# Kernel tuning notes

Hardware: AMD Instinct MI355X
Metric: run time of the kernel (lower is better)

The kernel has to match this reference:

```python
import jax, jax.numpy as jnp
import numpy as np

B, C, N, K, H = 8, 32, 4096, 32, 4  # batch, d_model, num_points, knn, heads
D = C // H
LN_EPS = 1e-5
ATT_EPS = 1e-6


def setup_inputs() -> dict:
    key = jax.random.key(0)
    ks = jax.random.split(key, 12)
    s = 0.05
    return {
        "search_feat": jax.random.normal(ks[0], (B, C, N), jnp.float32),
        "search_xyz": jax.random.normal(ks[1], (B, N, 3), jnp.float32),
        # pos MLP: Linear(3,32)+ReLU+Linear(32,32), weights stored [in,out]
        "w_pos1": jax.random.normal(ks[2], (3, 32), jnp.float32) * s,
        "b_pos1": jnp.zeros((32,), jnp.float32),
        "w_pos2": jax.random.normal(ks[3], (32, 32), jnp.float32) * s,
        "b_pos2": jnp.zeros((32,), jnp.float32),
        "w_q": jax.random.normal(ks[4], (C, C), jnp.float32) * s,
        "w_k": jax.random.normal(ks[5], (C, C), jnp.float32) * s,
        "w_v": jax.random.normal(ks[6], (C, C), jnp.float32) * s,
        "w_merge": jax.random.normal(ks[7], (C, C), jnp.float32) * s,
        "ln1_g": jnp.ones((C,), jnp.float32),
        "ln1_b": jnp.zeros((C,), jnp.float32),
        "w_mlp1": jax.random.normal(ks[8], (2 * C, 2 * C), jnp.float32) * s,
        "w_mlp2": jax.random.normal(ks[9], (2 * C, C), jnp.float32) * s,
        "ln2_g": jnp.ones((C,), jnp.float32),
        "ln2_b": jnp.zeros((C,), jnp.float32),
    }


def _layernorm(x, g, b):
    m = jnp.mean(x, axis=-1, keepdims=True)
    v = jnp.mean((x - m) ** 2, axis=-1, keepdims=True)
    return g * (x - m) * jax.lax.rsqrt(v + LN_EPS) + b


def _elu1(x):
    return jax.nn.elu(x) + 1.0


def reference(search_feat, search_xyz, w_pos1, b_pos1, w_pos2, b_pos2,
              w_q, w_k, w_v, w_merge, ln1_g, ln1_b, w_mlp1, w_mlp2,
              ln2_g, ln2_b):
    b, c, n = search_feat.shape
    h, d, k = H, C // H, K

    xt = jnp.transpose(search_feat, (0, 2, 1))  # [B,N,C]
    # knn in feature space: pd = -||xi||^2 + 2 xi.xj - ||xj||^2 (neg sq dist)
    xx = jnp.sum(xt * xt, axis=-1)  # [B,N]
    pd = 2.0 * jnp.einsum('bnc,bmc->bnm', xt, xt) - xx[:, :, None] - xx[:, None, :]
    idx = jax.lax.top_k(pd, k)[1]  # [B,N,K] nearest (incl. self)

    gather = jax.vmap(lambda f, i: f[i])  # per-batch gather
    fea_knn = gather(xt, idx)            # [B,N,K,C]
    xyz_knn = gather(search_xyz, idx)    # [B,N,K,3]

    def pos_mlp(z):
        return jax.nn.relu(z @ w_pos1 + b_pos1) @ w_pos2 + b_pos2

    q_in = xt + pos_mlp(search_xyz)      # [B,N,C]  (query, L=1)
    kv_in = fea_knn + pos_mlp(xyz_knn)   # [B,N,K,C]

    Q = (q_in @ w_q).reshape(b, n, h, d)          # [B,N,H,D]
    Ky = (kv_in @ w_k).reshape(b, n, k, h, d)     # [B,N,K,H,D]
    V = (kv_in @ w_v).reshape(b, n, k, h, d)

    Qf = _elu1(Q)
    Kf = _elu1(Ky)
    Vn = V / k  # v_length = K
    KV = jnp.einsum('bnkhd,bnkhv->bnhdv', Kf, Vn)
    Z = 1.0 / (jnp.einsum('bnhd,bnhd->bnh', Qf, Kf.sum(axis=2)) + ATT_EPS)
    msg = jnp.einsum('bnhd,bnhdv,bnh->bnhv', Qf, KV, Z) * k  # [B,N,H,D]

    msg = msg.reshape(b, n, c) @ w_merge
    msg = _layernorm(msg, ln1_g, ln1_b)
    msg = jnp.concatenate([xt, msg], axis=-1)          # [B,N,2C]
    msg = jax.nn.relu(msg @ w_mlp1) @ w_mlp2           # [B,N,C]
    msg = _layernorm(msg, ln2_g, ln2_b)
    return jnp.transpose(xt + msg, (0, 2, 1))          # [B,C,N]
```

## Files before the change

kernel.cpp:

```cpp
#include <hip/hip_runtime.h>
#include <math.h>

#define BB 8
#define CC 32
#define NN 4096
#define KNN 32
#define NP (BB*NN)

#define OFF_XT  0u
#define OFF_QF  1048576u
#define OFF_KV  2097152u
#define OFF_XX  4194304u
#define OFF_IDX 4227072u
#define OFF_XH  5275648u
#define OFF_XL  5799936u
#define OFF_MSG 5275648u

typedef _Float16 f16x8 __attribute__((ext_vector_type(8)));
typedef float f32x4 __attribute__((ext_vector_type(4)));
#define MFMA16(A,B,C) __builtin_amdgcn_mfma_f32_16x16x32_f16(A,B,C,0,0,0)

__device__ __forceinline__ float elu1(float x) {
    return x > 0.f ? x + 1.f : expf(x);
}

__global__ __launch_bounds__(256) void k_transpose(const float* __restrict__ feat,
                                                   float* __restrict__ xt,
                                                   _Float16* __restrict__ Xh,
                                                   _Float16* __restrict__ Xl,
                                                   float* __restrict__ xx) {
    __shared__ float tile[32][65];
    int b = blockIdx.y;
    int n0 = blockIdx.x * 64;
    int t = threadIdx.x;
    int nn = t & 63, cr = t >> 6;
#pragma unroll
    for (int r = 0; r < 8; ++r) {
        int c = r * 4 + cr;
        tile[c][nn] = feat[((size_t)b * 32 + c) * NN + n0 + nn];
    }
    __syncthreads();
    int c2 = t & 31, nr = t >> 5;
#pragma unroll
    for (int r = 0; r < 8; ++r) {
        int nl = r * 8 + nr;
        size_t gi = ((size_t)b * NN + n0 + nl) * 32 + c2;
        float v = tile[c2][nl];
        xt[gi] = v;
        _Float16 hv = (_Float16)v;
        Xh[gi] = hv;
        Xl[gi] = (_Float16)(v - (float)hv);
    }
    if (t < 64) {
        float s = 0.f;
#pragma unroll
        for (int c = 0; c < 32; ++c) { float u = tile[c][t]; s += u * u; }
        xx[(size_t)b * NN + n0 + t] = s;
    }
}

__global__ __launch_bounds__(256, 2) void k_prep(
        const float* __restrict__ xt, const float* __restrict__ xyz,
        const float* __restrict__ w_pos1, const float* __restrict__ b_pos1,
        const float* __restrict__ w_pos2, const float* __restrict__ b_pos2,
        const float* __restrict__ w_q, const float* __restrict__ w_k,
        const float* __restrict__ w_v,
        float* __restrict__ Qf, float* __restrict__ KV) {
    __shared__ float sW2[1024], sWq[1024], sWk[1024], sWv[1024];
    int t = threadIdx.x;
    for (int i = t; i < 1024; i += 256) {
        sW2[i] = w_pos2[i];
        sWq[i] = w_q[i];
        sWk[i] = w_k[i];
        sWv[i] = w_v[i];
    }
    int lane = t & 31;
    int g = t >> 5;
    float w1c0 = w_pos1[lane], w1c1 = w_pos1[32 + lane], w1c2 = w_pos1[64 + lane];
    float b1c = b_pos1[lane], b2c = b_pos2[lane];
    __syncthreads();
#pragma unroll 1
    for (int p = blockIdx.x * 8 + g; p < NP; p += gridDim.x * 8) {
        asm volatile("" ::: "memory");
        float x0 = xyz[(size_t)p * 3 + 0];
        float x1 = xyz[(size_t)p * 3 + 1];
        float x2 = xyz[(size_t)p * 3 + 2];
        float h = fmaxf(x0 * w1c0 + x1 * w1c1 + x2 * w1c2 + b1c, 0.f);
        float P = b2c;
#pragma unroll 8
        for (int j = 0; j < 32; ++j) P += __shfl(h, j, 32) * sW2[j * 32 + lane];
        float xv = xt[(size_t)p * 32 + lane];
        float qin = xv + P;
        float qa = 0.f, ka = 0.f, va = 0.f;
#pragma unroll 8
        for (int j = 0; j < 32; ++j) {
            float qj = __shfl(qin, j, 32);
            qa += qj * sWq[j * 32 + lane];
            ka += qj * sWk[j * 32 + lane];
            va += qj * sWv[j * 32 + lane];
        }
        Qf[(size_t)p * 32 + lane] = elu1(qa);
        float2 kvv;
        kvv.x = elu1(ka);
        kvv.y = va;
        *(((float2*)(KV + (size_t)p * 64)) + lane) = kvv;
    }
}

__global__ __launch_bounds__(256, 4) void k_knn(
        const _Float16* __restrict__ Xh, const _Float16* __restrict__ Xl,
        const float* __restrict__ xt, const float* __restrict__ xx,
        unsigned* __restrict__ idxg) {
    __shared__ unsigned histU[32 * 132];
    __shared__ unsigned outIdx[32][32];
    __shared__ unsigned tieIdx[32][96];
    __shared__ int sT[32];
    __shared__ unsigned sBase[32];
    __shared__ float sFloor[32];
    __shared__ unsigned outCnt[32], tieCnt[32];
    __shared__ float sM2;
    __shared__ float redbuf[4];

    int bid = blockIdx.x;
    int b = bid & 7;
    int n0 = (bid >> 3) << 5;
    int t = threadIdx.x;
    int lane = t & 63, wv = t >> 6;
    size_t bbase = (size_t)b * NN;

    for (int i = t; i < 32 * 132; i += 256) histU[i] = 0u;
    if (t < 32) { outCnt[t] = 0u; tieCnt[t] = 0u; }

    float lm = 0.f;
    for (int i = t; i < NN; i += 256) lm = fmaxf(lm, xx[bbase + i]);
#pragma unroll
    for (int off = 32; off >= 1; off >>= 1) lm = fmaxf(lm, __shfl_xor(lm, off, 64));
    if (lane == 0) redbuf[wv] = lm;
    __syncthreads();
    if (t == 0) sM2 = fmaxf(fmaxf(redbuf[0], redbuf[1]), fmaxf(redbuf[2], redbuf[3]));
    __syncthreads();
    float M2 = sM2;

    int al = lane & 15;
    int kgrp = lane >> 4;
    int ak = kgrp * 8;
    const _Float16* Xhb = Xh + bbase * 32;
    const _Float16* Xlb = Xl + bbase * 32;
    const float* xxb = xx + bbase;
    f16x8 Ah0 = *(const f16x8*)(Xhb + (size_t)(n0 + al) * 32 + ak);
    f16x8 Al0 = *(const f16x8*)(Xlb + (size_t)(n0 + al) * 32 + ak);
    f16x8 Ah1 = *(const f16x8*)(Xhb + (size_t)(n0 + 16 + al) * 32 + ak);
    f16x8 Al1 = *(const f16x8*)(Xlb + (size_t)(n0 + 16 + al) * 32 + ak);

    const float C127 = 127.99f;
    float sc2[8], scn[8], c0a[8];
    unsigned rowW[8];
    int rowloc8[8];
#pragma unroll
    for (int r = 0; r < 8; ++r) {
        int rowloc = (r < 4 ? 0 : 16) + kgrp * 4 + (r & 3);
        float xxi = xxb[n0 + rowloc];
        float scale = C127 / (2.f * (xxi + M2));
        sc2[r] = scale + scale;
        scn[r] = -scale;
        c0a[r] = __builtin_fmaf(-xxi, scale, C127);
        rowW[r] = (unsigned)rowloc * 132u;
        rowloc8[r] = rowloc;
    }

    unsigned cp0 = (unsigned)(wv * 1024 + al);
    unsigned akB = (unsigned)ak * 2u;
    const char* XhbB = (const char*)Xhb;
    const char* XlbB = (const char*)Xlb;

#pragma unroll 1
    for (int tt = 0; tt < 8; ++tt) {
        unsigned cp = cp0 + (unsigned)(tt << 4);
        f16x8 Bh = *(const f16x8*)(XhbB + cp * 64u + akB);
        f16x8 Bl = *(const f16x8*)(XlbB + cp * 64u + akB);
        float xxj = xxb[cp];
        f32x4 z = {0.f, 0.f, 0.f, 0.f};
        f32x4 u0 = MFMA16(Al0, Bl, z); u0 = MFMA16(Ah0, Bl, u0);
        f32x4 w0 = MFMA16(Al0, Bh, z); w0 = MFMA16(Ah0, Bh, w0);
        f32x4 u1 = MFMA16(Al1, Bl, z); u1 = MFMA16(Ah1, Bl, u1);
        f32x4 w1 = MFMA16(Al1, Bh, z); w1 = MFMA16(Ah1, Bh, w1);
#pragma unroll
        for (int r = 0; r < 8; ++r) {
            float a = (r < 4) ? (u0[r] + w0[r]) : (u1[r - 4] + w1[r - 4]);
            float bcol = __builtin_fmaf(xxj, scn[r], c0a[r]);
            float qf = __builtin_fmaf(a, sc2[r], bcol);
            float qc = __builtin_amdgcn_fmed3f(qf, 0.f, C127);
            atomicAdd(&histU[rowW[r] + (unsigned)qc], 1u);
        }
    }
    __syncthreads();

#pragma unroll 1
    for (int rr = 0; rr < 8; ++rr) {
        int row = wv * 8 + rr;
        const unsigned* Hr = histU + row * 132;
        unsigned cl = Hr[2 * lane], ch = Hr[2 * lane + 1];
        unsigned ss = cl + ch;
        unsigned acc = ss;
#pragma unroll
        for (int off = 1; off < 64; off <<= 1) {
            unsigned vv = __shfl_down(acc, off, 64);
            if (lane + off < 64) acc += vv;
        }
        unsigned run = acc - ss;
        int Tl = -1;
        if (run < 32u && run + ch >= 32u) Tl = 2 * lane + 1;
        run += ch;
        if (Tl < 0 && run < 32u && run + cl >= 32u) Tl = 2 * lane;
        unsigned long long bal = __ballot(Tl >= 0);
        int src = __ffsll(bal) - 1;
        int Tv = __shfl(Tl, src, 64);
        if (lane == 0) sFloor[row] = (Tv <= 0) ? -3.0e38f : (float)Tv;
    }
    __syncthreads();

    float fb1[8];
#pragma unroll
    for (int r = 0; r < 8; ++r) fb1[r] = sFloor[rowloc8[r]];

    {
        unsigned cpc = cp0 + (8u << 4);
        f16x8 Bh_c = *(const f16x8*)(XhbB + cpc * 64u + akB);
        f16x8 Bl_c = *(const f16x8*)(XlbB + cpc * 64u + akB);
        float xxj_c = xxb[cpc];
#pragma unroll 1
        for (int tt = 8; tt < 64; ++tt) {
            int tn = (tt + 1 < 64) ? (tt + 1) : 8;
            unsigned cpn = cp0 + (unsigned)(tn << 4);
            f16x8 Bh_n = *(const f16x8*)(XhbB + cpn * 64u + akB);
            f16x8 Bl_n = *(const f16x8*)(XlbB + cpn * 64u + akB);
            float xxj_n = xxb[cpn];
            f32x4 z = {0.f, 0.f, 0.f, 0.f};
            f32x4 u0 = MFMA16(Al0, Bl_c, z); u0 = MFMA16(Ah0, Bl_c, u0);
            f32x4 w0 = MFMA16(Al0, Bh_c, z); w0 = MFMA16(Ah0, Bh_c, w0);
            f32x4 u1 = MFMA16(Al1, Bl_c, z); u1 = MFMA16(Ah1, Bl_c, u1);
            f32x4 w1 = MFMA16(Al1, Bh_c, z); w1 = MFMA16(Ah1, Bh_c, w1);
            float bcol[8];
#pragma unroll
            for (int r = 0; r < 8; ++r) bcol[r] = __builtin_fmaf(xxj_c, scn[r], c0a[r]);
#pragma unroll
            for (int r = 0; r < 8; ++r) {
                float a = (r < 4) ? (u0[r] + w0[r]) : (u1[r - 4] + w1[r - 4]);
                float qf = __builtin_fmaf(a, sc2[r], bcol[r]);
                if (qf >= fb1[r]) {
                    float qc = __builtin_amdgcn_fmed3f(qf, 0.f, C127);
                    atomicAdd(&histU[rowW[r] + (unsigned)qc], 1u);
                }
            }
            Bh_c = Bh_n; Bl_c = Bl_n; xxj_c = xxj_n;
        }
    }
    __syncthreads();

#pragma unroll 1
    for (int rr = 0; rr < 8; ++rr) {
        int row = wv * 8 + rr;
        const unsigned* Hr = histU + row * 132;
        unsigned cl = Hr[2 * lane], ch = Hr[2 * lane + 1];
        unsigned ss = cl + ch;
        unsigned acc = ss;
#pragma unroll
        for (int off = 1; off < 64; off <<= 1) {
            unsigned vv = __shfl_down(acc, off, 64);
            if (lane + off < 64) acc += vv;
        }
        unsigned run = acc - ss;
        int Tl = -1; unsigned bl = 0;
        if (run < 32u && run + ch >= 32u) { Tl = 2 * lane + 1; bl = run; }
        run += ch;
        if (Tl < 0 && run < 32u && run + cl >= 32u) { Tl = 2 * lane; bl = run; }
        unsigned long long bal = __ballot(Tl >= 0);
        int src = __ffsll(bal) - 1;
        int Tv = __shfl(Tl, src, 64);
        unsigned bv = (unsigned)__shfl((int)bl, src, 64);
        if (lane == 0) { sT[row] = Tv; sBase[row] = bv; }
    }
    __syncthreads();

    float Tin[8], Tlo[8];
#pragma unroll
    for (int r = 0; r < 8; ++r) {
        int T = sT[rowloc8[r]];
        Tin[r] = (float)(T + 1);
        Tlo[r] = (T == 0) ? -3.0e38f : (float)T;
    }

    {
        f16x8 Bh_c = *(const f16x8*)(XhbB + cp0 * 64u + akB);
        f16x8 Bl_c = *(const f16x8*)(XlbB + cp0 * 64u + akB);
        float xxj_c = xxb[cp0];
#pragma unroll 1
        for (int tt = 0; tt < 64; ++tt) {
            unsigned cp = cp0 + (unsigned)(tt << 4);
            unsigned cpn = cp0 + (unsigned)(((tt + 1) & 63) << 4);
            f16x8 Bh_n = *(const f16x8*)(XhbB + cpn * 64u + akB);
            f16x8 Bl_n = *(const f16x8*)(XlbB + cpn * 64u + akB);
            float xxj_n = xxb[cpn];
            f32x4 z = {0.f, 0.f, 0.f, 0.f};
            f32x4 u0 = MFMA16(Al0, Bl_c, z); u0 = MFMA16(Ah0, Bl_c, u0);
            f32x4 w0 = MFMA16(Al0, Bh_c, z); w0 = MFMA16(Ah0, Bh_c, w0);
            f32x4 u1 = MFMA16(Al1, Bl_c, z); u1 = MFMA16(Ah1, Bl_c, u1);
            f32x4 w1 = MFMA16(Al1, Bh_c, z); w1 = MFMA16(Ah1, Bh_c, w1);
            float bcol[8];
#pragma unroll
            for (int r = 0; r < 8; ++r) bcol[r] = __builtin_fmaf(xxj_c, scn[r], c0a[r]);
#pragma unroll
            for (int r = 0; r < 8; ++r) {
                float a = (r < 4) ? (u0[r] + w0[r]) : (u1[r - 4] + w1[r - 4]);
                float qf = __builtin_fmaf(a, sc2[r], bcol[r]);
                if (qf >= Tlo[r]) {
                    unsigned row = rowW[r] / 132u;
                    if (qf >= Tin[r]) {
                        unsigned pos = atomicAdd(&outCnt[row], 1u);
                        outIdx[row][pos] = cp;
                    } else {
                        unsigned tp = atomicAdd(&tieCnt[row], 1u);
                        if (tp < 96u) tieIdx[row][tp] = cp;
                    }
                }
            }
            Bh_c = Bh_n; Bl_c = Bl_n; xxj_c = xxj_n;
        }
    }
    __syncthreads();

#pragma unroll 1
    for (int rr = 0; rr < 8; ++rr) {
        int row = wv * 8 + rr;
        int gr = n0 + row;
        unsigned bA = sBase[row];
        int need = 32 - (int)bA;
        if (need <= 0) continue;
        int nt = (int)tieCnt[row]; if (nt > 96) nt = 96;
        const float* xr = xt + (bbase + gr) * 32;
        float xxi_r = xxb[gr];
        float v0 = -INFINITY, v1 = -INFINITY;
        int i0 = 0x7fffffff, i1 = 0x7fffffff;
        bool a0v = lane < nt, a1v = lane + 64 < nt;
        if (a0v) {
            int c = (int)tieIdx[row][lane];
            const float* xc = xt + (bbase + c) * 32;
            float dot = 0.f;
#pragma unroll
            for (int ch = 0; ch < 32; ch += 4) {
                float4 rv = *(const float4*)(xr + ch);
                float4 cv = *(const float4*)(xc + ch);
                dot = __builtin_fmaf(rv.x, cv.x, dot);
                dot = __builtin_fmaf(rv.y, cv.y, dot);
                dot = __builtin_fmaf(rv.z, cv.z, dot);
                dot = __builtin_fmaf(rv.w, cv.w, dot);
            }
            v0 = 2.f * dot - xxi_r - xxb[c];
            i0 = c;
        }
        if (a1v) {
            int c = (int)tieIdx[row][lane + 64];
            const float* xc = xt + (bbase + c) * 32;
            float dot = 0.f;
#pragma unroll
            for (int ch = 0; ch < 32; ch += 4) {
                float4 rv = *(const float4*)(xr + ch);
                float4 cv = *(const float4*)(xc + ch);
                dot = __builtin_fmaf(rv.x, cv.x, dot);
                dot = __builtin_fmaf(rv.y, cv.y, dot);
                dot = __builtin_fmaf(rv.z, cv.z, dot);
                dot = __builtin_fmaf(rv.w, cv.w, dot);
            }
            v1 = 2.f * dot - xxi_r - xxb[c];
            i1 = c;
        }
        for (int it = 0; it < need; ++it) {
            float bvv = -INFINITY; int bj2 = 0x7fffffff;
            if (a0v && (v0 > bvv || (v0 == bvv && i0 < bj2))) { bvv = v0; bj2 = i0; }
            if (a1v && (v1 > bvv || (v1 == bvv && i1 < bj2))) { bvv = v1; bj2 = i1; }
#pragma unroll
            for (int off = 1; off < 64; off <<= 1) {
                float ov = __shfl_xor(bvv, off, 64);
                int oj = __shfl_xor(bj2, off, 64);
                if (ov > bvv || (ov == bvv && oj < bj2)) { bvv = ov; bj2 = oj; }
            }
            if (a0v && i0 == bj2) a0v = false;
            if (a1v && i1 == bj2) a1v = false;
            if (lane == 0) outIdx[row][bA + it] = (unsigned)bj2;
        }
    }
    __syncthreads();

    for (int i = t; i < 1024; i += 256)
        idxg[(bbase + n0 + (i >> 5)) * 32 + (i & 31)] = outIdx[i >> 5][i & 31];
}

__global__ __launch_bounds__(256) void k_attn(
        const float* __restrict__ Qf, const float* __restrict__ KV,
        const unsigned* __restrict__ idxg, float* __restrict__ msg) {
    int t = threadIdx.x;
    int wv = t >> 6, lane = t & 63;
    int l32 = lane & 31;
    int p = blockIdx.x * 8 + wv * 2 + (lane >> 5);
    int b = p >> 12;
    size_t bbase = (size_t)b * NN;
    const char* KVb = (const char*)(KV + bbase * 64);
    float q = Qf[(size_t)p * 32 + l32];
    int jv = (int)idxg[(size_t)p * 32 + l32];
    unsigned laneoff = (unsigned)l32 * 8u;
    float zacc = 0.f, macc = 0.f;
#pragma unroll 8
    for (int k = 0; k < 32; ++k) {
        int j = __shfl(jv, k, 32);
        unsigned off = ((unsigned)j << 8) + laneoff;
        float2 kv = *(const float2*)(KVb + off);
        float s = q * kv.x;
        s += __shfl_xor(s, 1, 8);
        s += __shfl_xor(s, 2, 8);
        s += __shfl_xor(s, 4, 8);
        zacc += s;
        macc = __builtin_fmaf(s, kv.y, macc);
    }
    float Z = 1.f / (zacc + 1e-6f);
    msg[(size_t)p * 32 + l32] = macc * Z;
}

__global__ __launch_bounds__(256, 2) void k_post(
        const float* __restrict__ msg, const float* __restrict__ xt,
        const float* __restrict__ w_merge,
        const float* __restrict__ ln1_g, const float* __restrict__ ln1_b,
        const float* __restrict__ w_mlp1, const float* __restrict__ w_mlp2,
        const float* __restrict__ ln2_g, const float* __restrict__ ln2_b,
        float* __restrict__ out) {
    __shared__ _Float16 wmT[2][32][32];
    __shared__ _Float16 w1T[2][64][64];
    __shared__ _Float16 w2T[2][32][64];
    __shared__ _Float16 sPh[4][16][40], sPl[4][16][40];
    __shared__ _Float16 sHh[4][16][72], sHl[4][16][72];
    int t = threadIdx.x;
    for (int i = t; i < 1024; i += 256) {
        float v = w_merge[i]; int in = i >> 5, o = i & 31;
        _Float16 h = (_Float16)v;
        wmT[0][o][in] = h; wmT[1][o][in] = (_Float16)(v - (float)h);
    }
    for (int i = t; i < 4096; i += 256) {
        float v = w_mlp1[i]; int in = i >> 6, o = i & 63;
        _Float16 h = (_Float16)v;
        w1T[0][o][in] = h; w1T[1][o][in] = (_Float16)(v - (float)h);
    }
    for (int i = t; i < 2048; i += 256) {
        float v = w_mlp2[i]; int in = i >> 5, o = i & 31;
        _Float16 h = (_Float16)v;
        w2T[0][o][in] = h; w2T[1][o][in] = (_Float16)(v - (float)h);
    }
    int wv = t >> 6, lane = t & 63;
    int row = lane & 15, kg = lane >> 4;
    int p0 = blockIdx.x * 64 + wv * 16;
    int b = p0 >> 12;
    float g1a = ln1_g[row], b1a = ln1_b[row], g1b = ln1_g[row + 16], b1b = ln1_b[row + 16];
    float g2a = ln2_g[row], b2a = ln2_b[row], g2b = ln2_g[row + 16], b2b = ln2_b[row + 16];
    __syncthreads();

    f32x4 z4 = {0.f, 0.f, 0.f, 0.f};
    f16x8 Amh, Aml;
    {
        const float* mr = msg + (size_t)(p0 + row) * 32 + kg * 8;
#pragma unroll
        for (int j = 0; j < 8; ++j) {
            float v = mr[j];
            _Float16 h = (_Float16)v;
            Amh[j] = h; Aml[j] = (_Float16)(v - (float)h);
        }
    }
    f32x4 accM[2];
#pragma unroll
    for (int n = 0; n < 2; ++n) {
        f16x8 Bh = *(const f16x8*)&wmT[0][n * 16 + row][kg * 8];
        f16x8 Bl = *(const f16x8*)&wmT[1][n * 16 + row][kg * 8];
        f32x4 a = z4;
        a = MFMA16(Aml, Bl, a); a = MFMA16(Amh, Bl, a);
        a = MFMA16(Aml, Bh, a); a = MFMA16(Amh, Bh, a);
        accM[n] = a;
    }
#pragma unroll
    for (int r = 0; r < 4; ++r) {
        float s0 = accM[0][r], s1 = accM[1][r];
        float sm = s0 + s1;
        sm += __shfl_xor(sm, 1, 64); sm += __shfl_xor(sm, 2, 64);
        sm += __shfl_xor(sm, 4, 64); sm += __shfl_xor(sm, 8, 64);
        float mean = sm * (1.f / 32.f);
        float d0 = s0 - mean, d1 = s1 - mean;
        float vv = d0 * d0 + d1 * d1;
        vv += __shfl_xor(vv, 1, 64); vv += __shfl_xor(vv, 2, 64);
        vv += __shfl_xor(vv, 4, 64); vv += __shfl_xor(vv, 8, 64);
        float rst = rsqrtf(vv * (1.f / 32.f) + 1e-5f);
        float m0 = g1a * d0 * rst + b1a;
        float m1 = g1b * d1 * rst + b1b;
        int pl = kg * 4 + r;
        _Float16 h0 = (_Float16)m0;
        sPh[wv][pl][row] = h0; sPl[wv][pl][row] = (_Float16)(m0 - (float)h0);
        _Float16 h1 = (_Float16)m1;
        sPh[wv][pl][row + 16] = h1; sPl[wv][pl][row + 16] = (_Float16)(m1 - (float)h1);
    }
    __syncthreads();
    f16x8 Axh, Axl;
    {
        const float* xr = xt + (size_t)(p0 + row) * 32 + kg * 8;
#pragma unroll
        for (int j = 0; j < 8; ++j) {
            float v = xr[j];
            _Float16 h = (_Float16)v;
            Axh[j] = h; Axl[j] = (_Float16)(v - (float)h);
        }
    }
    f16x8 Aph = *(const f16x8*)&sPh[wv][row][kg * 8];
    f16x8 Apl = *(const f16x8*)&sPl[wv][row][kg * 8];
    f32x4 accH[4];
#pragma unroll
    for (int n = 0; n < 4; ++n) {
        f16x8 B0h = *(const f16x8*)&w1T[0][n * 16 + row][kg * 8];
        f16x8 B0l = *(const f16x8*)&w1T[1][n * 16 + row][kg * 8];
        f16x8 B1h = *(const f16x8*)&w1T[0][n * 16 + row][32 + kg * 8];
        f16x8 B1l = *(const f16x8*)&w1T[1][n * 16 + row][32 + kg * 8];
        f32x4 a = z4;
        a = MFMA16(Axl, B0l, a); a = MFMA16(Axh, B0l, a);
        a = MFMA16(Axl, B0h, a); a = MFMA16(Axh, B0h, a);
        a = MFMA16(Apl, B1l, a); a = MFMA16(Aph, B1l, a);
        a = MFMA16(Apl, B1h, a); a = MFMA16(Aph, B1h, a);
        accH[n] = a;
    }
#pragma unroll
    for (int n = 0; n < 4; ++n) {
#pragma unroll
        for (int r = 0; r < 4; ++r) {
            float hv = fmaxf(accH[n][r], 0.f);
            int pl = kg * 4 + r;
            _Float16 hh = (_Float16)hv;
            sHh[wv][pl][n * 16 + row] = hh;
            sHl[wv][pl][n * 16 + row] = (_Float16)(hv - (float)hh);
        }
    }
    __syncthreads();
    f16x8 Hh0 = *(const f16x8*)&sHh[wv][row][kg * 8];
    f16x8 Hl0 = *(const f16x8*)&sHl[wv][row][kg * 8];
    f16x8 Hh1 = *(const f16x8*)&sHh[wv][row][32 + kg * 8];
    f16x8 Hl1 = *(const f16x8*)&sHl[wv][row][32 + kg * 8];
    f32x4 accO[2];
#pragma unroll
    for (int n = 0; n < 2; ++n) {
        f16x8 B0h = *(const f16x8*)&w2T[0][n * 16 + row][kg * 8];
        f16x8 B0l = *(const f16x8*)&w2T[1][n * 16 + row][kg * 8];
        f16x8 B1h = *(const f16x8*)&w2T[0][n * 16 + row][32 + kg * 8];
        f16x8 B1l = *(const f16x8*)&w2T[1][n * 16 + row][32 + kg * 8];
        f32x4 a = z4;
        a = MFMA16(Hl0, B0l, a); a = MFMA16(Hh0, B0l, a);
        a = MFMA16(Hl0, B0h, a); a = MFMA16(Hh0, B0h, a);
        a = MFMA16(Hl1, B1l, a); a = MFMA16(Hh1, B1l, a);
        a = MFMA16(Hl1, B1h, a); a = MFMA16(Hh1, B1h, a);
        accO[n] = a;
    }
#pragma unroll
    for (int r = 0; r < 4; ++r) {
        float s0 = accO[0][r], s1 = accO[1][r];
        float sm = s0 + s1;
        sm += __shfl_xor(sm, 1, 64); sm += __shfl_xor(sm, 2, 64);
        sm += __shfl_xor(sm, 4, 64); sm += __shfl_xor(sm, 8, 64);
        float mean = sm * (1.f / 32.f);
        float d0 = s0 - mean, d1 = s1 - mean;
        float vv = d0 * d0 + d1 * d1;
        vv += __shfl_xor(vv, 1, 64); vv += __shfl_xor(vv, 2, 64);
        vv += __shfl_xor(vv, 4, 64); vv += __shfl_xor(vv, 8, 64);
        float rst = rsqrtf(vv * (1.f / 32.f) + 1e-5f);
        float o0 = g2a * d0 * rst + b2a;
        float o1 = g2b * d1 * rst + b2b;
        int pt = p0 + kg * 4 + r;
        int nb = pt & 4095;
        float xv0 = xt[(size_t)pt * 32 + row];
        float xv1 = xt[(size_t)pt * 32 + row + 16];
        out[((size_t)b * 32 + row) * 4096 + nb] = xv0 + o0;
        out[((size_t)b * 32 + row + 16) * 4096 + nb] = xv1 + o1;
    }
}

extern "C" void kernel_launch(void* const* d_in, const int* in_sizes, int n_in,
                              void* d_out, int out_size, void* d_ws, size_t ws_size,
                              hipStream_t stream) {
    const float* feat   = (const float*)d_in[0];
    const float* xyz    = (const float*)d_in[1];
    const float* w_pos1 = (const float*)d_in[2];
    const float* b_pos1 = (const float*)d_in[3];
    const float* w_pos2 = (const float*)d_in[4];
    const float* b_pos2 = (const float*)d_in[5];
    const float* w_q    = (const float*)d_in[6];
    const float* w_k    = (const float*)d_in[7];
    const float* w_v    = (const float*)d_in[8];
    const float* w_mg   = (const float*)d_in[9];
    const float* ln1_g  = (const float*)d_in[10];
    const float* ln1_b  = (const float*)d_in[11];
    const float* w_mlp1 = (const float*)d_in[12];
    const float* w_mlp2 = (const float*)d_in[13];
    const float* ln2_g  = (const float*)d_in[14];
    const float* ln2_b  = (const float*)d_in[15];
    float* ws = (float*)d_ws;
    float* xt = ws + OFF_XT;
    float* Qf = ws + OFF_QF;
    float* KVp = ws + OFF_KV;
    float* xx = ws + OFF_XX;
    unsigned* idxg = (unsigned*)(ws + OFF_IDX);
    _Float16* Xh = (_Float16*)(ws + OFF_XH);
    _Float16* Xl = (_Float16*)(ws + OFF_XL);
    float* msg = ws + OFF_MSG;
    float* out = (float*)d_out;

    k_transpose<<<dim3(64, 8), 256, 0, stream>>>(feat, xt, Xh, Xl, xx);
    k_prep<<<1024, 256, 0, stream>>>(xt, xyz, w_pos1, b_pos1, w_pos2, b_pos2,
                                     w_q, w_k, w_v, Qf, KVp);
    k_knn<<<1024, 256, 0, stream>>>(Xh, Xl, xt, xx, idxg);
    k_attn<<<4096, 256, 0, stream>>>(Qf, KVp, idxg, msg);
    k_post<<<512, 256, 0, stream>>>(msg, xt, w_mg, ln1_g, ln1_b,
                                    w_mlp1, w_mlp2, ln2_g, ln2_b, out);
}
```

Before: 242.8 us.

## Fuse KNN refinement and selection passes using a candidate buffer

Restructures the histogram-based top-k selection in the KNN kernel. It widens the full sample pass from 8 to 24 tiles, then runs a single pass over all columns that stores candidates above the floor, as packed index plus bucket, into a shared buffer while finishing the histogram. The exact threshold is then computed from the histogram, and the buffered candidates are split into sure picks and ties without recomputing the MFMA distances. This removes one full distance-recompute pass over N. In exchange it uses more LDS, lowers launch bounds occupancy to 2, and silently drops candidates beyond 192 per row, which can break correctness if the floor is loose. Buffered candidates are never re-synced before the tie pass reads cand and outCnt; each row is owned by a single wave, so this likely works.

```diff
diff --git a/kernel.cpp b/kernel.cpp
--- a/kernel.cpp
+++ b/kernel.cpp
@@ -107,17 +107,16 @@
     }
 }
 
-__global__ __launch_bounds__(256, 4) void k_knn(
+__global__ __launch_bounds__(256, 2) void k_knn(
         const _Float16* __restrict__ Xh, const _Float16* __restrict__ Xl,
         const float* __restrict__ xt, const float* __restrict__ xx,
         unsigned* __restrict__ idxg) {
-    __shared__ unsigned histU[32 * 132];
+    __shared__ unsigned histU[32 * 129];
+    __shared__ unsigned cand[32][192];
     __shared__ unsigned outIdx[32][32];
-    __shared__ unsigned tieIdx[32][96];
     __shared__ int sT[32];
-    __shared__ unsigned sBase[32];
     __shared__ float sFloor[32];
-    __shared__ unsigned outCnt[32], tieCnt[32];
+    __shared__ unsigned candCnt[32], outCnt[32], tieCnt[32];
     __shared__ float sM2;
     __shared__ float redbuf[4];
 
@@ -128,8 +127,8 @@
     int lane = t & 63, wv = t >> 6;
     size_t bbase = (size_t)b * NN;
 
-    for (int i = t; i < 32 * 132; i += 256) histU[i] = 0u;
-    if (t < 32) { outCnt[t] = 0u; tieCnt[t] = 0u; }
+    for (int i = t; i < 32 * 129; i += 256) histU[i] = 0u;
+    if (t < 32) { candCnt[t] = 0u; outCnt[t] = 0u; tieCnt[t] = 0u; }
 
     float lm = 0.f;
     for (int i = t; i < NN; i += 256) lm = fmaxf(lm, xx[bbase + i]);
@@ -164,7 +163,7 @@
         sc2[r] = scale + scale;
         scn[r] = -scale;
         c0a[r] = __builtin_fmaf(-xxi, scale, C127);
-        rowW[r] = (unsigned)rowloc * 132u;
+        rowW[r] = (unsigned)rowloc * 129u;
         rowloc8[r] = rowloc;
     }
 
@@ -173,24 +172,31 @@
     const char* XhbB = (const char*)Xhb;
     const char* XlbB = (const char*)Xlb;
 
+    {
+        f16x8 Bh_c = *(const f16x8*)(XhbB + cp0 * 64u + akB);
+        f16x8 Bl_c = *(const f16x8*)(XlbB + cp0 * 64u + akB);
+        float xxj_c = xxb[cp0];
 #pragma unroll 1
-    for (int tt = 0; tt < 8; ++tt) {
-        unsigned cp = cp0 + (unsigned)(tt << 4);
-        f16x8 Bh = *(const f16x8*)(XhbB + cp * 64u + akB);
-        f16x8 Bl = *(const f16x8*)(XlbB + cp * 64u + akB);
-        float xxj = xxb[cp];
-        f32x4 z = {0.f, 0.f, 0.f, 0.f};
-        f32x4 u0 = MFMA16(Al0, Bl, z); u0 = MFMA16(Ah0, Bl, u0);
-        f32x4 w0 = MFMA16(Al0, Bh, z); w0 = MFMA16(Ah0, Bh, w0);
-        f32x4 u1 = MFMA16(Al1, Bl, z); u1 = MFMA16(Ah1, Bl, u1);
-        f32x4 w1 = MFMA16(Al1, Bh, z); w1 = MFMA16(Ah1, Bh, w1);
-#pragma unroll
-        for (int r = 0; r < 8; ++r) {
-            float a = (r < 4) ? (u0[r] + w0[r]) : (u1[r - 4] + w1[r - 4]);
-            float bcol = __builtin_fmaf(xxj, scn[r], c0a[r]);
-            float qf = __builtin_fmaf(a, sc2[r], bcol);
-            float qc = __builtin_amdgcn_fmed3f(qf, 0.f, C127);
-            atomicAdd(&histU[rowW[r] + (unsigned)qc], 1u);
+        for (int tt = 0; tt < 24; ++tt) {
+            int tn = (tt + 1 < 24) ? (tt + 1) : 0;
+            unsigned cpn = cp0 + (unsigned)(tn << 4);
+            f16x8 Bh_n = *(const f16x8*)(XhbB + cpn * 64u + akB);
+            f16x8 Bl_n = *(const f16x8*)(XlbB + cpn * 64u + akB);
+            float xxj_n = xxb[cpn];
+            f32x4 z = {0.f, 0.f, 0.f, 0.f};
+            f32x4 u0 = MFMA16(Al0, Bl_c, z); u0 = MFMA16(Ah0, Bl_c, u0);
+            f32x4 w0 = MFMA16(Al0, Bh_c, z); w0 = MFMA16(Ah0, Bh_c, w0);
+            f32x4 u1 = MFMA16(Al1, Bl_c, z); u1 = MFMA16(Ah1, Bl_c, u1);
+            f32x4 w1 = MFMA16(Al1, Bh_c, z); w1 = MFMA16(Ah1, Bh_c, w1);
+#pragma unroll
+            for (int r = 0; r < 8; ++r) {
+                float a = (r < 4) ? (u0[r] + w0[r]) : (u1[r - 4] + w1[r - 4]);
+                float bcol = __builtin_fmaf(xxj_c, scn[r], c0a[r]);
+                float qf = __builtin_fmaf(a, sc2[r], bcol);
+                float qc = __builtin_amdgcn_fmed3f(qf, 0.f, C127);
+                atomicAdd(&histU[rowW[r] + (unsigned)qc], 1u);
+            }
+            Bh_c = Bh_n; Bl_c = Bl_n; xxj_c = xxj_n;
         }
     }
     __syncthreads();
@@ -198,7 +204,7 @@
 #pragma unroll 1
     for (int rr = 0; rr < 8; ++rr) {
         int row = wv * 8 + rr;
-        const unsigned* Hr = histU + row * 132;
+        const unsigned* Hr = histU + row * 129;
         unsigned cl = Hr[2 * lane], ch = Hr[2 * lane + 1];
         unsigned ss = cl + ch;
         unsigned acc = ss;
@@ -222,73 +228,6 @@
     float fb1[8];
 #pragma unroll
     for (int r = 0; r < 8; ++r) fb1[r] = sFloor[rowloc8[r]];
-
-    {
-        unsigned cpc = cp0 + (8u << 4);
-        f16x8 Bh_c = *(const f16x8*)(XhbB + cpc * 64u + akB);
-        f16x8 Bl_c = *(const f16x8*)(XlbB + cpc * 64u + akB);
-        float xxj_c = xxb[cpc];
-#pragma unroll 1
-        for (int tt = 8; tt < 64; ++tt) {
-            int tn = (tt + 1 < 64) ? (tt + 1) : 8;
-            unsigned cpn = cp0 + (unsigned)(tn << 4);
-            f16x8 Bh_n = *(const f16x8*)(XhbB + cpn * 64u + akB);
-            f16x8 Bl_n = *(const f16x8*)(XlbB + cpn * 64u + akB);
-            float xxj_n = xxb[cpn];
-            f32x4 z = {0.f, 0.f, 0.f, 0.f};
-            f32x4 u0 = MFMA16(Al0, Bl_c, z); u0 = MFMA16(Ah0, Bl_c, u0);
-            f32x4 w0 = MFMA16(Al0, Bh_c, z); w0 = MFMA16(Ah0, Bh_c, w0);
-            f32x4 u1 = MFMA16(Al1, Bl_c, z); u1 = MFMA16(Ah1, Bl_c, u1);
-            f32x4 w1 = MFMA16(Al1, Bh_c, z); w1 = MFMA16(Ah1, Bh_c, w1);
-            float bcol[8];
-#pragma unroll
-            for (int r = 0; r < 8; ++r) bcol[r] = __builtin_fmaf(xxj_c, scn[r], c0a[r]);
-#pragma unroll
-            for (int r = 0; r < 8; ++r) {
-                float a = (r < 4) ? (u0[r] + w0[r]) : (u1[r - 4] + w1[r - 4]);
-                float qf = __builtin_fmaf(a, sc2[r], bcol[r]);
-                if (qf >= fb1[r]) {
-                    float qc = __builtin_amdgcn_fmed3f(qf, 0.f, C127);
-                    atomicAdd(&histU[rowW[r] + (unsigned)qc], 1u);
-                }
-            }
-            Bh_c = Bh_n; Bl_c = Bl_n; xxj_c = xxj_n;
-        }
-    }
-    __syncthreads();
-
-#pragma unroll 1
-    for (int rr = 0; rr < 8; ++rr) {
-        int row = wv * 8 + rr;
-        const unsigned* Hr = histU + row * 132;
-        unsigned cl = Hr[2 * lane], ch = Hr[2 * lane + 1];
-        unsigned ss = cl + ch;
-        unsigned acc = ss;
-#pragma unroll
-        for (int off = 1; off < 64; off <<= 1) {
-            unsigned vv = __shfl_down(acc, off, 64);
-            if (lane + off < 64) acc += vv;
-        }
-        unsigned run = acc - ss;
-        int Tl = -1; unsigned bl = 0;
-        if (run < 32u && run + ch >= 32u) { Tl = 2 * lane + 1; bl = run; }
-        run += ch;
-        if (Tl < 0 && run < 32u && run + cl >= 32u) { Tl = 2 * lane; bl = run; }
-        unsigned long long bal = __ballot(Tl >= 0);
-        int src = __ffsll(bal) - 1;
-        int Tv = __shfl(Tl, src, 64);
-        unsigned bv = (unsigned)__shfl((int)bl, src, 64);
-        if (lane == 0) { sT[row] = Tv; sBase[row] = bv; }
-    }
-    __syncthreads();
-
-    float Tin[8], Tlo[8];
-#pragma unroll
-    for (int r = 0; r < 8; ++r) {
-        int T = sT[rowloc8[r]];
-        Tin[r] = (float)(T + 1);
-        Tlo[r] = (T == 0) ? -3.0e38f : (float)T;
-    }
 
     {
         f16x8 Bh_c = *(const f16x8*)(XhbB + cp0 * 64u + akB);
@@ -309,31 +248,78 @@
             float bcol[8];
 #pragma unroll
             for (int r = 0; r < 8; ++r) bcol[r] = __builtin_fmaf(xxj_c, scn[r], c0a[r]);
+            bool dohist = (tt >= 24);
 #pragma unroll
             for (int r = 0; r < 8; ++r) {
                 float a = (r < 4) ? (u0[r] + w0[r]) : (u1[r - 4] + w1[r - 4]);
                 float qf = __builtin_fmaf(a, sc2[r], bcol[r]);
-                if (qf >= Tlo[r]) {
-                    unsigned row = rowW[r] / 132u;
-                    if (qf >= Tin[r]) {
-                        unsigned pos = atomicAdd(&outCnt[row], 1u);
-                        outIdx[row][pos] = cp;
-                    } else {
-                        unsigned tp = atomicAdd(&tieCnt[row], 1u);
-                        if (tp < 96u) tieIdx[row][tp] = cp;
-                    }
+                if (qf >= fb1[r]) {
+                    float qc = __builtin_amdgcn_fmed3f(qf, 0.f, C127);
+                    unsigned bkt = (unsigned)qc;
+                    unsigned row = (unsigned)rowloc8[r];
+                    unsigned pos = atomicAdd(&candCnt[row], 1u);
+                    if (pos < 192u) cand[row][pos] = (cp << 8) | bkt;
+                    if (dohist) atomicAdd(&histU[rowW[r] + bkt], 1u);
                 }
             }
             Bh_c = Bh_n; Bl_c = Bl_n; xxj_c = xxj_n;
         }
     }
     __syncthreads();
+
+#pragma unroll 1
+    for (int rr = 0; rr < 8; ++rr) {
+        int row = wv * 8 + rr;
+        const unsigned* Hr = histU + row * 129;
+        unsigned cl = Hr[2 * lane], ch = Hr[2 * lane + 1];
+        unsigned ss = cl + ch;
+        unsigned acc = ss;
+#pragma unroll
+        for (int off = 1; off < 64; off <<= 1) {
+            unsigned vv = __shfl_down(acc, off, 64);
+            if (lane + off < 64) acc += vv;
+        }
+        unsigned run = acc - ss;
+        int Tl = -1;
+        if (run < 32u && run + ch >= 32u) Tl = 2 * lane + 1;
+        run += ch;
+        if (Tl < 0 && run < 32u && run + cl >= 32u) Tl = 2 * lane;
+        unsigned long long bal = __ballot(Tl >= 0);
+        int src = __ffsll(bal) - 1;
+        int Tv = __shfl(Tl, src, 64);
+        if (lane == 0) sT[row] = Tv;
+    }
+    __syncthreads();
+
+#pragma unroll 1
+    for (int rr = 0; rr < 8; ++rr) {
+        int row = wv * 8 + rr;
+        int T = sT[row];
+        int nc = (int)candCnt[row]; if (nc > 192) nc = 192;
+        unsigned e0 = (lane < nc) ? cand[row][lane] : 0xffffffffu;
+        unsigned e1 = (lane + 64 < nc) ? cand[row][lane + 64] : 0xffffffffu;
+        unsigned e2 = (lane + 128 < nc) ? cand[row][lane + 128] : 0xffffffffu;
+#pragma unroll
+        for (int q = 0; q < 3; ++q) {
+            unsigned e = (q == 0) ? e0 : (q == 1) ? e1 : e2;
+            if (e != 0xffffffffu) {
+                int bk = (int)(e & 255u);
+                if (bk > T) {
+                    unsigned pos = atomicAdd(&outCnt[row], 1u);
+                    outIdx[row][pos] = e >> 8;
+                } else if (bk == T) {
+                    unsigned tp = atomicAdd(&tieCnt[row], 1u);
+                    if (tp < 96u) cand[row][tp] = e >> 8;
+                }
+            }
+        }
+    }
 
 #pragma unroll 1
     for (int rr = 0; rr < 8; ++rr) {
         int row = wv * 8 + rr;
         int gr = n0 + row;
-        unsigned bA = sBase[row];
+        unsigned bA = outCnt[row];
         int need = 32 - (int)bA;
         if (need <= 0) continue;
         int nt = (int)tieCnt[row]; if (nt > 96) nt = 96;
@@ -343,7 +329,7 @@
         int i0 = 0x7fffffff, i1 = 0x7fffffff;
         bool a0v = lane < nt, a1v = lane + 64 < nt;
         if (a0v) {
-            int c = (int)tieIdx[row][lane];
+            int c = (int)cand[row][lane];
             const float* xc = xt + (bbase + c) * 32;
             float dot = 0.f;
 #pragma unroll
@@ -359,7 +345,7 @@
             i0 = c;
         }
         if (a1v) {
-            int c = (int)tieIdx[row][lane + 64];
+            int c = (int)cand[row][lane + 64];
             const float* xc = xt + (bbase + c) * 32;
             float dot = 0.f;
 #pragma unroll
```

Result: slower. 316.1 us (+30.2%).

## Use single fp16 MFMA for kNN distances with widened tie band

Applied to the files above, without the earlier changes.

Drops the hi/lo fp16 split of the features and computes kNN dot products with one fp16 MFMA per tile instead of four, removing the Xl buffer and its loads. To absorb the lower precision, the candidate band around the threshold bucket is widened by a margin. Borderline candidates are then resolved by the existing exact fp32 tie refinement. The base count now comes from outCnt instead of the histogram prefix. This risks more tie candidates, possible overflow of the 96-entry tie buffer, or misclassified neighbors if the fp16 error exceeds the margin.

```diff
diff --git a/kernel.cpp b/kernel.cpp
--- a/kernel.cpp
+++ b/kernel.cpp
@@ -13,8 +13,7 @@
 #define OFF_XX  4194304u
 #define OFF_IDX 4227072u
 #define OFF_XH  5275648u
-#define OFF_XL  5799936u
-#define OFF_MSG 5275648u
+#define OFF_MSG 5799936u
 
 typedef _Float16 f16x8 __attribute__((ext_vector_type(8)));
 typedef float f32x4 __attribute__((ext_vector_type(4)));
@@ -27,7 +26,6 @@
 __global__ __launch_bounds__(256) void k_transpose(const float* __restrict__ feat,
                                                    float* __restrict__ xt,
                                                    _Float16* __restrict__ Xh,
-                                                   _Float16* __restrict__ Xl,
                                                    float* __restrict__ xx) {
     __shared__ float tile[32][65];
     int b = blockIdx.y;
@@ -47,9 +45,7 @@
         size_t gi = ((size_t)b * NN + n0 + nl) * 32 + c2;
         float v = tile[c2][nl];
         xt[gi] = v;
-        _Float16 hv = (_Float16)v;
-        Xh[gi] = hv;
-        Xl[gi] = (_Float16)(v - (float)hv);
+        Xh[gi] = (_Float16)v;
     }
     if (t < 64) {
         float s = 0.f;
@@ -108,14 +104,13 @@
 }
 
 __global__ __launch_bounds__(256, 4) void k_knn(
-        const _Float16* __restrict__ Xh, const _Float16* __restrict__ Xl,
+        const _Float16* __restrict__ Xh,
         const float* __restrict__ xt, const float* __restrict__ xx,
         unsigned* __restrict__ idxg) {
     __shared__ unsigned histU[32 * 132];
     __shared__ unsigned outIdx[32][32];
     __shared__ unsigned tieIdx[32][96];
     __shared__ int sT[32];
-    __shared__ unsigned sBase[32];
     __shared__ float sFloor[32];
     __shared__ unsigned outCnt[32], tieCnt[32];
     __shared__ float sM2;
@@ -145,12 +140,9 @@
     int kgrp = lane >> 4;
     int ak = kgrp * 8;
     const _Float16* Xhb = Xh + bbase * 32;
-    const _Float16* Xlb = Xl + bbase * 32;
     const float* xxb = xx + bbase;
     f16x8 Ah0 = *(const f16x8*)(Xhb + (size_t)(n0 + al) * 32 + ak);
-    f16x8 Al0 = *(const f16x8*)(Xlb + (size_t)(n0 + al) * 32 + ak);
     f16x8 Ah1 = *(const f16x8*)(Xhb + (size_t)(n0 + 16 + al) * 32 + ak);
-    f16x8 Al1 = *(const f16x8*)(Xlb + (size_t)(n0 + 16 + al) * 32 + ak);
 
     const float C127 = 127.99f;
     float sc2[8], scn[8], c0a[8];
@@ -171,22 +163,18 @@
     unsigned cp0 = (unsigned)(wv * 1024 + al);
     unsigned akB = (unsigned)ak * 2u;
     const char* XhbB = (const char*)Xhb;
-    const char* XlbB = (const char*)Xlb;
+    const f32x4 z = {0.f, 0.f, 0.f, 0.f};
 
 #pragma unroll 1
     for (int tt = 0; tt < 8; ++tt) {
         unsigned cp = cp0 + (unsigned)(tt << 4);
         f16x8 Bh = *(const f16x8*)(XhbB + cp * 64u + akB);
-        f16x8 Bl = *(const f16x8*)(XlbB + cp * 64u + akB);
         float xxj = xxb[cp];
-        f32x4 z = {0.f, 0.f, 0.f, 0.f};
-        f32x4 u0 = MFMA16(Al0, Bl, z); u0 = MFMA16(Ah0, Bl, u0);
-        f32x4 w0 = MFMA16(Al0, Bh, z); w0 = MFMA16(Ah0, Bh, w0);
-        f32x4 u1 = MFMA16(Al1, Bl, z); u1 = MFMA16(Ah1, Bl, u1);
-        f32x4 w1 = MFMA16(Al1, Bh, z); w1 = MFMA16(Ah1, Bh, w1);
+        f32x4 a0 = MFMA16(Ah0, Bh, z);
+        f32x4 a1 = MFMA16(Ah1, Bh, z);
 #pragma unroll
         for (int r = 0; r < 8; ++r) {
-            float a = (r < 4) ? (u0[r] + w0[r]) : (u1[r - 4] + w1[r - 4]);
+            float a = (r < 4) ? a0[r] : a1[r - 4];
             float bcol = __builtin_fmaf(xxj, scn[r], c0a[r]);
             float qf = __builtin_fmaf(a, sc2[r], bcol);
             float qc = __builtin_amdgcn_fmed3f(qf, 0.f, C127);
@@ -226,33 +214,28 @@
     {
         unsigned cpc = cp0 + (8u << 4);
         f16x8 Bh_c = *(const f16x8*)(XhbB + cpc * 64u + akB);
-        f16x8 Bl_c = *(const f16x8*)(XlbB + cpc * 64u + akB);
         float xxj_c = xxb[cpc];
 #pragma unroll 1
         for (int tt = 8; tt < 64; ++tt) {
             int tn = (tt + 1 < 64) ? (tt + 1) : 8;
             unsigned cpn = cp0 + (unsigned)(tn << 4);
             f16x8 Bh_n = *(const f16x8*)(XhbB + cpn * 64u + akB);
-            f16x8 Bl_n = *(const f16x8*)(XlbB + cpn * 64u + akB);
             float xxj_n = xxb[cpn];
-            f32x4 z = {0.f, 0.f, 0.f, 0.f};
-            f32x4 u0 = MFMA16(Al0, Bl_c, z); u0 = MFMA16(Ah0, Bl_c, u0);
-            f32x4 w0 = MFMA16(Al0, Bh_c, z); w0 = MFMA16(Ah0, Bh_c, w0);
-            f32x4 u1 = MFMA16(Al1, Bl_c, z); u1 = MFMA16(Ah1, Bl_c, u1);
-            f32x4 w1 = MFMA16(Al1, Bh_c, z); w1 = MFMA16(Ah1, Bh_c, w1);
+            f32x4 a0 = MFMA16(Ah0, Bh_c, z);
+            f32x4 a1 = MFMA16(Ah1, Bh_c, z);
             float bcol[8];
 #pragma unroll
             for (int r = 0; r < 8; ++r) bcol[r] = __builtin_fmaf(xxj_c, scn[r], c0a[r]);
 #pragma unroll
             for (int r = 0; r < 8; ++r) {
-                float a = (r < 4) ? (u0[r] + w0[r]) : (u1[r - 4] + w1[r - 4]);
+                float a = (r < 4) ? a0[r] : a1[r - 4];
                 float qf = __builtin_fmaf(a, sc2[r], bcol[r]);
                 if (qf >= fb1[r]) {
                     float qc = __builtin_amdgcn_fmed3f(qf, 0.f, C127);
                     atomicAdd(&histU[rowW[r] + (unsigned)qc], 1u);
                 }
             }
-            Bh_c = Bh_n; Bl_c = Bl_n; xxj_c = xxj_n;
+            Bh_c = Bh_n; xxj_c = xxj_n;
         }
     }
     __syncthreads();
@@ -270,15 +253,14 @@
             if (lane + off < 64) acc += vv;
         }
         unsigned run = acc - ss;
-        int Tl = -1; unsigned bl = 0;
-        if (run < 32u && run + ch >= 32u) { Tl = 2 * lane + 1; bl = run; }
+        int Tl = -1;
+        if (run < 32u && run + ch >= 32u) Tl = 2 * lane + 1;
         run += ch;
-        if (Tl < 0 && run < 32u && run + cl >= 32u) { Tl = 2 * lane; bl = run; }
+        if (Tl < 0 && run < 32u && run + cl >= 32u) Tl = 2 * lane;
         unsigned long long bal = __ballot(Tl >= 0);
         int src = __ffsll(bal) - 1;
         int Tv = __shfl(Tl, src, 64);
-        unsigned bv = (unsigned)__shfl((int)bl, src, 64);
-        if (lane == 0) { sT[row] = Tv; sBase[row] = bv; }
+        if (lane == 0) sT[row] = Tv;
     }
     __syncthreads();
 
@@ -286,35 +268,30 @@
 #pragma unroll
     for (int r = 0; r < 8; ++r) {
         int T = sT[rowloc8[r]];
-        Tin[r] = (float)(T + 1);
-        Tlo[r] = (T == 0) ? -3.0e38f : (float)T;
+        Tin[r] = (float)(T + 1) + 0.1875f;
+        Tlo[r] = (T == 0) ? -3.0e38f : ((float)T - 0.1875f);
     }
 
     {
         f16x8 Bh_c = *(const f16x8*)(XhbB + cp0 * 64u + akB);
-        f16x8 Bl_c = *(const f16x8*)(XlbB + cp0 * 64u + akB);
         float xxj_c = xxb[cp0];
 #pragma unroll 1
         for (int tt = 0; tt < 64; ++tt) {
             unsigned cp = cp0 + (unsigned)(tt << 4);
             unsigned cpn = cp0 + (unsigned)(((tt + 1) & 63) << 4);
             f16x8 Bh_n = *(const f16x8*)(XhbB + cpn * 64u + akB);
-            f16x8 Bl_n = *(const f16x8*)(XlbB + cpn * 64u + akB);
             float xxj_n = xxb[cpn];
-            f32x4 z = {0.f, 0.f, 0.f, 0.f};
-            f32x4 u0 = MFMA16(Al0, Bl_c, z); u0 = MFMA16(Ah0, Bl_c, u0);
-            f32x4 w0 = MFMA16(Al0, Bh_c, z); w0 = MFMA16(Ah0, Bh_c, w0);
-            f32x4 u1 = MFMA16(Al1, Bl_c, z); u1 = MFMA16(Ah1, Bl_c, u1);
-            f32x4 w1 = MFMA16(Al1, Bh_c, z); w1 = MFMA16(Ah1, Bh_c, w1);
+            f32x4 a0 = MFMA16(Ah0, Bh_c, z);
+            f32x4 a1 = MFMA16(Ah1, Bh_c, z);
             float bcol[8];
 #pragma unroll
             for (int r = 0; r < 8; ++r) bcol[r] = __builtin_fmaf(xxj_c, scn[r], c0a[r]);
 #pragma unroll
             for (int r = 0; r < 8; ++r) {
-                float a = (r < 4) ? (u0[r] + w0[r]) : (u1[r - 4] + w1[r - 4]);
+                float a = (r < 4) ? a0[r] : a1[r - 4];
                 float qf = __builtin_fmaf(a, sc2[r], bcol[r]);
                 if (qf >= Tlo[r]) {
-                    unsigned row = rowW[r] / 132u;
+                    unsigned row = (unsigned)rowloc8[r];
                     if (qf >= Tin[r]) {
                         unsigned pos = atomicAdd(&outCnt[row], 1u);
                         outIdx[row][pos] = cp;
@@ -324,7 +301,7 @@
                     }
                 }
             }
-            Bh_c = Bh_n; Bl_c = Bl_n; xxj_c = xxj_n;
+            Bh_c = Bh_n; xxj_c = xxj_n;
         }
     }
     __syncthreads();
@@ -333,7 +310,7 @@
     for (int rr = 0; rr < 8; ++rr) {
         int row = wv * 8 + rr;
         int gr = n0 + row;
-        unsigned bA = sBase[row];
+        unsigned bA = outCnt[row];
         int need = 32 - (int)bA;
         if (need <= 0) continue;
         int nt = (int)tieCnt[row]; if (nt > 96) nt = 96;
@@ -608,14 +585,13 @@
     float* xx = ws + OFF_XX;
     unsigned* idxg = (unsigned*)(ws + OFF_IDX);
     _Float16* Xh = (_Float16*)(ws + OFF_XH);
-    _Float16* Xl = (_Float16*)(ws + OFF_XL);
     float* msg = ws + OFF_MSG;
     float* out = (float*)d_out;
 
-    k_transpose<<<dim3(64, 8), 256, 0, stream>>>(feat, xt, Xh, Xl, xx);
+    k_transpose<<<dim3(64, 8), 256, 0, stream>>>(feat, xt, Xh, xx);
     k_prep<<<1024, 256, 0, stream>>>(xt, xyz, w_pos1, b_pos1, w_pos2, b_pos2,
                                      w_q, w_k, w_v, Qf, KVp);
-    k_knn<<<1024, 256, 0, stream>>>(Xh, Xl, xt, xx, idxg);
+    k_knn<<<1024, 256, 0, stream>>>(Xh, xt, xx, idxg);
     k_attn<<<4096, 256, 0, stream>>>(Qf, KVp, idxg, msg);
     k_post<<<512, 256, 0, stream>>>(msg, xt, w_mg, ln1_g, ln1_b,
                                     w_mlp1, w_mlp2, ln2_g, ln2_b, out);
```

Result: faster. 234.6 us (median of 2 runs) (-3.4%).
